# Kernel optimization log

Measured on AMD Instinct MI355X. Metric: run time of the kernel, lower is better.

## Reference

```python
import jax, jax.numpy as jnp
import numpy as np

N_NODES = 100000
N_EDGES = 640000
WIDTH = 128
LAYERS = 3
N_GRAPHS = 64


def setup_inputs() -> dict:
    key = jax.random.key(0)
    ks = jax.random.split(key, 6)
    x = jax.random.normal(ks[0], (N_NODES, WIDTH), dtype=jnp.float32)
    edge_index = jax.random.randint(ks[1], (2, N_EDGES), 0, N_NODES, dtype=jnp.int64)
    edge_attr = jax.random.uniform(ks[2], (N_EDGES, 1), dtype=jnp.float32)
    batch = jnp.sort(jax.random.randint(ks[3], (N_NODES,), 0, N_GRAPHS, dtype=jnp.int64))
    Ws = jax.random.normal(ks[4], (LAYERS, WIDTH, WIDTH), dtype=jnp.float32) / np.sqrt(WIDTH)
    bs = jnp.zeros((LAYERS, WIDTH), dtype=jnp.float32)
    return {"x": x, "edge_index": edge_index, "edge_attr": edge_attr,
            "batch": batch, "Ws": Ws, "bs": bs}


def reference(x, edge_index, edge_attr, batch, Ws, bs):
    N = x.shape[0]
    ew = edge_attr.squeeze()  # [E]
    loop = jnp.arange(N)
    # add self-loops with fill_value=2.0 (improved=True)
    row = jnp.concatenate([edge_index[0], loop])
    col = jnp.concatenate([edge_index[1], loop])
    w = jnp.concatenate([ew, jnp.full((N,), 2.0, dtype=ew.dtype)])
    # symmetric gcn normalization: deg computed at target (col)
    deg = jax.ops.segment_sum(w, col, num_segments=N)
    dinv = jnp.where(deg > 0, jax.lax.rsqrt(deg), 0.0)
    norm = dinv[row] * w * dinv[col]  # [E+N]

    for l in range(LAYERS):
        h = x @ Ws[l]  # [N, WIDTH]
        msg = norm[:, None] * h[row]  # gather + scale
        x = jax.ops.segment_sum(msg, col, num_segments=N) + bs[l]

    # global mean pool over graphs
    sums = jax.ops.segment_sum(x, batch, num_segments=N_GRAPHS)
    counts = jax.ops.segment_sum(jnp.ones((N,), dtype=x.dtype), batch, num_segments=N_GRAPHS)
    return sums / jnp.maximum(counts, 1.0)[:, None]
```

## Files before the change

kernel.cpp:

```cpp
#include <hip/hip_runtime.h>
#include <hip/hip_fp16.h>
#include <cstddef>

#define N_NODES  100000
#define N_EDGES  640000
#define WIDTH    128
#define LAYERS   3
#define N_GRAPHS 64
#define ELL_K    40

__device__ __forceinline__ float h2f(unsigned short h) {
  __half x; *reinterpret_cast<unsigned short*>(&x) = h;
  return __half2float(x);
}
__device__ __forceinline__ unsigned short f2h(float f) {
  __half h = __float2half_rn(f);
  return *reinterpret_cast<unsigned short*>(&h);
}


__global__ void k_init(int* __restrict__ cursor, float* __restrict__ deg) {
  int i = blockIdx.x * blockDim.x + threadIdx.x;
  if (i < N_NODES) { cursor[i] = 0; deg[i] = 0.f; }
}

__global__ void k_fill_cd(const int* __restrict__ row, const int* __restrict__ col,
                          const float* __restrict__ ew,
                          int* __restrict__ cursor, float* __restrict__ deg,
                          int2* __restrict__ ell) {
  int e = blockIdx.x * blockDim.x + threadIdx.x;
  if (e < N_EDGES) {
    int r = row[e], c = col[e];
    float w = ew[e];
    atomicAdd(&deg[c], w);
    int slot = atomicAdd(&cursor[r], 1);
    if (slot < ELL_K) {
      int2 pk; pk.x = c; pk.y = __float_as_int(w);
      ell[(size_t)r * ELL_K + slot] = pk;
    }
  }
}

__global__ void k_dinv_e(const float* __restrict__ deg, float* __restrict__ dinv,
                         float* __restrict__ d2, float* __restrict__ sq) {
  int v = blockIdx.x * blockDim.x + threadIdx.x;
  if (v < N_NODES) {
    float d = 2.0f + deg[v];
    float di = (d > 0.0f) ? 1.0f / sqrtf(d) : 0.0f;
    dinv[v] = di;
    d2[v] = di * di;
    sq[v] = sqrtf(d);
  }
}

__device__ __forceinline__ int lbound(const int* __restrict__ batch, int key) {
  int lo = 0, hi = N_NODES;
  while (lo < hi) { int m = (lo + hi) >> 1; if (batch[m] < key) lo = m + 1; else hi = m; }
  return lo;
}

__global__ void k_cntg(const int* __restrict__ batch, int* __restrict__ cntg,
                       float* __restrict__ invc) {
  int g = threadIdx.x;
  if (g < N_GRAPHS) {
    int lb = lbound(batch, g), ub = lbound(batch, g + 1);
    int c = ub - lb;
    cntg[g] = c;
    invc[g] = 1.0f / (float)max(c, 1);
  }
}

__global__ void k_pinit(const int* __restrict__ batch, const float* __restrict__ invc,
                        const float* __restrict__ dinv, unsigned short* __restrict__ p) {
  const int total = N_NODES * 16;
  for (int i = blockIdx.x * blockDim.x + threadIdx.x; i < total;
       i += gridDim.x * blockDim.x) {
    int v = i >> 4, q = i & 15;
    int b = batch[v];
    unsigned short val = f2h(invc[b] * dinv[v]);
    ushort4 u;
    ((unsigned short*)&u)[0] = (q * 4 + 0 == b) ? val : (unsigned short)0;
    ((unsigned short*)&u)[1] = (q * 4 + 1 == b) ? val : (unsigned short)0;
    ((unsigned short*)&u)[2] = (q * 4 + 2 == b) ? val : (unsigned short)0;
    ((unsigned short*)&u)[3] = (q * 4 + 3 == b) ? val : (unsigned short)0;
    ((ushort4*)p)[i] = u;
  }
}

#define CS_BLOCKS 512
__global__ __launch_bounds__(256) void k_colsum(
    const unsigned short* __restrict__ y, const float* __restrict__ sq,
    float* __restrict__ partc) {
  __shared__ float4 sd[256];
  int t = threadIdx.x;
  int slot = t & 15;
  int vrow = t >> 4;
  const int chunk = (N_NODES + CS_BLOCKS - 1) / CS_BLOCKS;
  int start = blockIdx.x * chunk;
  int end = min(start + chunk, N_NODES);
  float4 acc = {0.f, 0.f, 0.f, 0.f};
  for (int v = start + vrow; v < end; v += 16) {
    ushort4 u = ((const ushort4*)(y + (size_t)v * 64))[slot];
    float rd = sq[v];
    acc.x += h2f(u.x) * rd; acc.y += h2f(u.y) * rd;
    acc.z += h2f(u.z) * rd; acc.w += h2f(u.w) * rd;
  }
  sd[t] = acc;
  __syncthreads();
  for (int off = 8; off > 0; off >>= 1) {
    if (vrow < off) {
      float4 o = sd[(vrow + off) * 16 + slot];
      acc.x += o.x; acc.y += o.y; acc.z += o.z; acc.w += o.w;
      sd[t] = acc;
    }
    __syncthreads();
  }
  if (vrow == 0)
    ((float4*)(partc + (size_t)blockIdx.x * 64))[slot] = acc;
}

__global__ __launch_bounds__(256) void k_cs2(
    const float* __restrict__ csA, const float* __restrict__ csB,
    float* __restrict__ ps, float* __restrict__ pas) {
  __shared__ float sd[256];
  const float* src = (blockIdx.x == 0) ? csA : csB;
  float* dst = (blockIdx.x == 0) ? ps : pas;
  int t = threadIdx.x;
  int g = t & 63, c = t >> 6;
  float a = 0.f;
  for (int r = c * 128; r < (c + 1) * 128; r++) a += src[r * 64 + g];
  sd[t] = a;
  __syncthreads();
  if (t < 128) sd[t] += sd[t + 128];
  __syncthreads();
  if (t < 64) dst[t] = sd[t] + sd[t + 64];
}

#define AGG_NPB 4
__global__ __launch_bounds__(256) void k_yagg(
    const unsigned short* __restrict__ yin, const int* __restrict__ cnt_a,
    const int2* __restrict__ ell, const float* __restrict__ scale,
    unsigned short* __restrict__ yout) {
  int wave = threadIdx.x >> 6;
  int lane = threadIdx.x & 63;
  int v = blockIdx.x * AGG_NPB + wave;
  if (v >= N_NODES) return;
  int vv = __builtin_amdgcn_readfirstlane(v);
  int grp = lane >> 4;
  int q = lane & 15;

  ushort4 hvu = ((const ushort4*)(yin + (size_t)vv * 64))[q];
  int cnt = cnt_a[vv];

  float4 a0 = {0,0,0,0}, a1 = {0,0,0,0}, a2 = {0,0,0,0}, a3 = {0,0,0,0};
  int2 pk = (lane < cnt) ? ell[(size_t)vv * ELL_K + lane] : make_int2(0, 0);
  int   si = pk.x;
  float swv = __int_as_float(pk.y);

  for (int base = 0; base < cnt; base += 16) {
    int e0 = base + grp;
    float w0 = __shfl(swv, e0); int i0 = __shfl(si, e0);
    ushort4 u0 = ((const ushort4*)(yin + (size_t)i0 * 64))[q];
    a0.x += w0 * h2f(u0.x); a0.y += w0 * h2f(u0.y);
    a0.z += w0 * h2f(u0.z); a0.w += w0 * h2f(u0.w);
    if (base + 4 < cnt) {
      int e1 = base + 4 + grp;
      float w1 = __shfl(swv, e1); int i1 = __shfl(si, e1);
      ushort4 u1 = ((const ushort4*)(yin + (size_t)i1 * 64))[q];
      a1.x += w1 * h2f(u1.x); a1.y += w1 * h2f(u1.y);
      a1.z += w1 * h2f(u1.z); a1.w += w1 * h2f(u1.w);
    }
    if (base + 8 < cnt) {
      int e2 = base + 8 + grp;
      int e3 = base + 12 + grp;
      float w2 = __shfl(swv, e2); int i2 = __shfl(si, e2);
      float w3 = __shfl(swv, e3); int i3 = __shfl(si, e3);
      ushort4 u2 = ((const ushort4*)(yin + (size_t)i2 * 64))[q];
      ushort4 u3 = ((const ushort4*)(yin + (size_t)i3 * 64))[q];
      a2.x += w2 * h2f(u2.x); a2.y += w2 * h2f(u2.y);
      a2.z += w2 * h2f(u2.z); a2.w += w2 * h2f(u2.w);
      a3.x += w3 * h2f(u3.x); a3.y += w3 * h2f(u3.y);
      a3.z += w3 * h2f(u3.z); a3.w += w3 * h2f(u3.w);
    }
  }

  a0.x += a1.x + a2.x + a3.x;
  a0.y += a1.y + a2.y + a3.y;
  a0.z += a1.z + a2.z + a3.z;
  a0.w += a1.w + a2.w + a3.w;
#pragma unroll
  for (int d = 16; d <= 32; d <<= 1) {
    a0.x += __shfl_xor(a0.x, d);
    a0.y += __shfl_xor(a0.y, d);
    a0.z += __shfl_xor(a0.z, d);
    a0.w += __shfl_xor(a0.w, d);
  }

  if (grp == 0) {
    float sc = scale[vv];
    ushort4 r;
    r.x = f2h(sc * (a0.x + 2.0f * h2f(hvu.x)));
    r.y = f2h(sc * (a0.y + 2.0f * h2f(hvu.y)));
    r.z = f2h(sc * (a0.z + 2.0f * h2f(hvu.z)));
    r.w = f2h(sc * (a0.w + 2.0f * h2f(hvu.w)));
    ((ushort4*)(yout + (size_t)vv * 64))[q] = r;
  }
}

#define CT_BLOCKS 1024

__global__ __launch_bounds__(256) void k_contract(
    const float* __restrict__ x0, const unsigned short* __restrict__ y3,
    float* __restrict__ part) {
  int t = threadIdx.x;
  int jq = t & 31;
  int gg = t >> 5;

  float4 acc[8];
#pragma unroll
  for (int i = 0; i < 8; i++) acc[i] = make_float4(0.f, 0.f, 0.f, 0.f);

  int v = blockIdx.x;
  for (; v + CT_BLOCKS < N_NODES; v += 2 * CT_BLOCKS) {
    int v2 = v + CT_BLOCKS;
    float4 xa = ((const float4*)(x0 + (size_t)v * WIDTH))[jq];
    float4 xb = ((const float4*)(x0 + (size_t)v2 * WIDTH))[jq];
    const ushort4* ya = (const ushort4*)(y3 + (size_t)v * 64 + gg * 8);
    const ushort4* yb = (const ushort4*)(y3 + (size_t)v2 * 64 + gg * 8);
    ushort4 ua0 = ya[0], ua1 = ya[1];
    ushort4 ub0 = yb[0], ub1 = yb[1];
    float yas[8] = {h2f(ua0.x), h2f(ua0.y), h2f(ua0.z), h2f(ua0.w),
                    h2f(ua1.x), h2f(ua1.y), h2f(ua1.z), h2f(ua1.w)};
    float ybs[8] = {h2f(ub0.x), h2f(ub0.y), h2f(ub0.z), h2f(ub0.w),
                    h2f(ub1.x), h2f(ub1.y), h2f(ub1.z), h2f(ub1.w)};
#pragma unroll
    for (int i = 0; i < 8; i++) {
      acc[i].x += yas[i] * xa.x; acc[i].y += yas[i] * xa.y;
      acc[i].z += yas[i] * xa.z; acc[i].w += yas[i] * xa.w;
    }
#pragma unroll
    for (int i = 0; i < 8; i++) {
      acc[i].x += ybs[i] * xb.x; acc[i].y += ybs[i] * xb.y;
      acc[i].z += ybs[i] * xb.z; acc[i].w += ybs[i] * xb.w;
    }
  }
  if (v < N_NODES) {
    float4 xa = ((const float4*)(x0 + (size_t)v * WIDTH))[jq];
    const ushort4* ya = (const ushort4*)(y3 + (size_t)v * 64 + gg * 8);
    ushort4 ua0 = ya[0], ua1 = ya[1];
    float yas[8] = {h2f(ua0.x), h2f(ua0.y), h2f(ua0.z), h2f(ua0.w),
                    h2f(ua1.x), h2f(ua1.y), h2f(ua1.z), h2f(ua1.w)};
#pragma unroll
    for (int i = 0; i < 8; i++) {
      acc[i].x += yas[i] * xa.x; acc[i].y += yas[i] * xa.y;
      acc[i].z += yas[i] * xa.z; acc[i].w += yas[i] * xa.w;
    }
  }

  float* dst = part + (size_t)blockIdx.x * (N_GRAPHS * WIDTH);
#pragma unroll
  for (int i = 0; i < 8; i++)
    *(float4*)(dst + (gg * 8 + i) * WIDTH + jq * 4) = acc[i];
}

#define RC_ROWS 64
#define RC_RG (CT_BLOCKS / RC_ROWS)

__global__ __launch_bounds__(256) void k_reduce1(
    const float* __restrict__ part, float* __restrict__ part2) {
  int bid = blockIdx.x, t = threadIdx.x;
  int rg = bid >> 5, colc = bid & 31;
  int idx = colc * 256 + t;
  const float* src = part + (size_t)rg * RC_ROWS * (N_GRAPHS * WIDTH) + idx;
  float a0 = 0.f, a1 = 0.f, a2 = 0.f, a3 = 0.f;
  for (int r = 0; r < RC_ROWS; r += 4) {
    a0 += src[(size_t)(r + 0) * (N_GRAPHS * WIDTH)];
    a1 += src[(size_t)(r + 1) * (N_GRAPHS * WIDTH)];
    a2 += src[(size_t)(r + 2) * (N_GRAPHS * WIDTH)];
    a3 += src[(size_t)(r + 3) * (N_GRAPHS * WIDTH)];
  }
  part2[rg * (N_GRAPHS * WIDTH) + idx] = (a0 + a1) + (a2 + a3);
}

__global__ __launch_bounds__(WIDTH) void k_mm128(
    const float* __restrict__ A, const float* __restrict__ B, float* __restrict__ O) {
  __shared__ float Ar[WIDTH];
  int r = blockIdx.x, j = threadIdx.x;
  Ar[j] = A[r * WIDTH + j];
  __syncthreads();
  float a = 0.f;
#pragma unroll 8
  for (int k = 0; k < WIDTH; k++) a += Ar[k] * B[k * WIDTH + j];
  O[r * WIDTH + j] = a;
}

__global__ __launch_bounds__(WIDTH) void k_c01(
    const float* __restrict__ b0, const float* __restrict__ T1,
    const float* __restrict__ b1, const float* __restrict__ W2,
    float* __restrict__ c0, float* __restrict__ c1) {
  __shared__ float s0[WIDTH], s1v[WIDTH];
  int j = threadIdx.x;
  s0[j] = b0[j]; s1v[j] = b1[j];
  __syncthreads();
  float a0 = 0.f, a1 = 0.f;
#pragma unroll 8
  for (int k = 0; k < WIDTH; k++) {
    a0 += s0[k] * T1[k * WIDTH + j];
    a1 += s1v[k] * W2[k * WIDTH + j];
  }
  c0[j] = a0; c1[j] = a1;
}

__global__ __launch_bounds__(WIDTH) void k_out(
    const float* __restrict__ part2, const float* __restrict__ Wp,
    const float* __restrict__ c0, const float* __restrict__ c1,
    const float* __restrict__ ps, const float* __restrict__ pas,
    const int* __restrict__ cntg, const float* __restrict__ b2,
    float* __restrict__ out) {
  __shared__ float Cr[WIDTH];
  int g = blockIdx.x, j = threadIdx.x;
  float cv = 0.f;
#pragma unroll
  for (int rg = 0; rg < RC_RG; rg++)
    cv += part2[rg * (N_GRAPHS * WIDTH) + g * WIDTH + j];
  Cr[j] = cv;
  __syncthreads();
  float a = pas[g] * c0[j] + ps[g] * c1[j] + ((cntg[g] > 0) ? b2[j] : 0.f);
#pragma unroll 8
  for (int k = 0; k < WIDTH; k++) a += Cr[k] * Wp[k * WIDTH + j];
  out[g * WIDTH + j] = a;
}


extern "C" void kernel_launch(void* const* d_in, const int* in_sizes, int n_in,
                              void* d_out, int out_size, void* d_ws, size_t ws_size,
                              hipStream_t stream) {
  const float* x   = (const float*)d_in[0];
  const int* row   = (const int*)d_in[1];
  const int* col   = row + N_EDGES;
  const float* ew  = (const float*)d_in[2];
  const int* batch = (const int*)d_in[3];
  const float* Ws  = (const float*)d_in[4];
  const float* bs  = (const float*)d_in[5];
  float* out = (float*)d_out;

  char* w = (char*)d_ws;
  float* dinv    = (float*)(w + 0);
  float* d2      = (float*)(w + 400128);
  float* sq      = (float*)(w + 800256);
  float* deg     = (float*)(w + 1200384);
  int*   cursor  = (int*)(w + 1600512);
  int*   cntg    = (int*)(w + 2000640);
  float* invc    = (float*)(w + 2000896);
  float* ps      = (float*)(w + 2001152);
  float* pas     = (float*)(w + 2001408);
  float* T1      = (float*)(w + 2001664);
  float* Wp      = (float*)(w + 2067200);
  float* c0      = (float*)(w + 2132736);
  float* c1      = (float*)(w + 2133248);
  int2*  ell     = (int2*)(w + 2133760);
  float* part    = (float*)(w + 34133760);
  float* part2   = (float*)(w + 67688192);
  unsigned short* yA = (unsigned short*)(w + 68212480);
  unsigned short* yB = (unsigned short*)(w + 81012480);
  float* csA     = (float*)(w + 93812480);
  float* csB     = (float*)(w + 93943552);

  int nb_n = (N_NODES + 255) / 256;
  int nb_e = (N_EDGES + 255) / 256;

  k_init   <<<nb_n, 256, 0, stream>>>(cursor, deg);
  k_fill_cd<<<nb_e, 256, 0, stream>>>(row, col, ew, cursor, deg, ell);
  k_dinv_e <<<nb_n, 256, 0, stream>>>(deg, dinv, d2, sq);

  k_cntg <<<1, 64, 0, stream>>>(batch, cntg, invc);
  k_pinit<<<2048, 256, 0, stream>>>(batch, invc, dinv, yA);

  int nb_y = (N_NODES + AGG_NPB - 1) / AGG_NPB;
  k_yagg  <<<nb_y, 256, 0, stream>>>(yA, cursor, ell, d2, yB);
  k_colsum<<<CS_BLOCKS, 256, 0, stream>>>(yB, sq, csA);
  k_yagg  <<<nb_y, 256, 0, stream>>>(yB, cursor, ell, d2, yA);
  k_colsum<<<CS_BLOCKS, 256, 0, stream>>>(yA, sq, csB);
  k_yagg  <<<nb_y, 256, 0, stream>>>(yA, cursor, ell, dinv, yB);

  k_cs2  <<<2, 256, 0, stream>>>(csA, csB, ps, pas);
  k_mm128<<<WIDTH, WIDTH, 0, stream>>>(Ws + 1 * WIDTH * WIDTH, Ws + 2 * WIDTH * WIDTH, T1);
  k_mm128<<<WIDTH, WIDTH, 0, stream>>>(Ws + 0 * WIDTH * WIDTH, T1, Wp);
  k_c01  <<<1, WIDTH, 0, stream>>>(bs, T1, bs + WIDTH, Ws + 2 * WIDTH * WIDTH, c0, c1);

  k_contract<<<CT_BLOCKS, 256, 0, stream>>>(x, yB, part);
  k_reduce1 <<<RC_RG * 32, 256, 0, stream>>>(part, part2);
  k_out     <<<N_GRAPHS, WIDTH, 0, stream>>>(part2, Wp, c0, c1, ps, pas, cntg,
                                             bs + 2 * WIDTH, out);
}
```

Measured before the change: 278.8 us.

## Stage contraction tiles in LDS via direct global-to-LDS loads

Restructures the contraction kernel so each block processes contiguous 64-node chunks. The x rows are loaded straight into shared memory with global_load_lds, and the fp16 y rows are converted to fp32 in shared memory before the FMA loop. Each thread now owns 16 graph-rows by 2 columns instead of 8 by 4, and the grid shrinks to 768 blocks. The aim is coalesced bulk loads and less per-node global traffic and conversion, at the cost of barriers, 48KB of LDS per block and lower occupancy. The reduce kernel's RC_RG still derives from CT_BLOCKS (now 768), so the partial-sum reduction must cope with the new block count.

Result: no change. 274.1 us (-1.7%).

```diff
diff --git a/kernel.cpp b/kernel.cpp
--- a/kernel.cpp
+++ b/kernel.cpp
@@ -8,6 +8,11 @@
 #define LAYERS   3
 #define N_GRAPHS 64
 #define ELL_K    40
+
+#define GLOAD_LDS16(gsrc, ldst) \
+  __builtin_amdgcn_global_load_lds( \
+      (const __attribute__((address_space(1))) unsigned*)(gsrc), \
+      (__attribute__((address_space(3))) unsigned*)(ldst), 16, 0, 0)
 
 __device__ __forceinline__ float h2f(unsigned short h) {
   __half x; *reinterpret_cast<unsigned short*>(&x) = h;
@@ -207,60 +212,93 @@
   }
 }
 
-#define CT_BLOCKS 1024
+#define CT_BLOCKS 768
+#define CT_NCHUNK ((N_NODES + 63) / 64)
 
 __global__ __launch_bounds__(256) void k_contract(
     const float* __restrict__ x0, const unsigned short* __restrict__ y3,
     float* __restrict__ part) {
+  __shared__ __align__(16) float xs[64 * 128];
+  __shared__ __align__(16) float ysf[64 * 64];
   int t = threadIdx.x;
-  int jq = t & 31;
-  int gg = t >> 5;
-
-  float4 acc[8];
-#pragma unroll
-  for (int i = 0; i < 8; i++) acc[i] = make_float4(0.f, 0.f, 0.f, 0.f);
-
-  int v = blockIdx.x;
-  for (; v + CT_BLOCKS < N_NODES; v += 2 * CT_BLOCKS) {
-    int v2 = v + CT_BLOCKS;
-    float4 xa = ((const float4*)(x0 + (size_t)v * WIDTH))[jq];
-    float4 xb = ((const float4*)(x0 + (size_t)v2 * WIDTH))[jq];
-    const ushort4* ya = (const ushort4*)(y3 + (size_t)v * 64 + gg * 8);
-    const ushort4* yb = (const ushort4*)(y3 + (size_t)v2 * 64 + gg * 8);
-    ushort4 ua0 = ya[0], ua1 = ya[1];
-    ushort4 ub0 = yb[0], ub1 = yb[1];
-    float yas[8] = {h2f(ua0.x), h2f(ua0.y), h2f(ua0.z), h2f(ua0.w),
-                    h2f(ua1.x), h2f(ua1.y), h2f(ua1.z), h2f(ua1.w)};
-    float ybs[8] = {h2f(ub0.x), h2f(ub0.y), h2f(ub0.z), h2f(ub0.w),
-                    h2f(ub1.x), h2f(ub1.y), h2f(ub1.z), h2f(ub1.w)};
+  int w = t >> 6;
+  int lane = t & 63;
+  int j = lane * 2;
+
+  float2 acc[16];
+#pragma unroll
+  for (int i = 0; i < 16; i++) acc[i] = make_float2(0.f, 0.f);
+
+  for (int c = blockIdx.x; c < CT_NCHUNK; c += gridDim.x) {
+    int cc = min(64, N_NODES - c * 64);
+    int bx = cc * 512;
+    int byh = cc * 128;
+    const char* gx = (const char*)(x0 + (size_t)c * 64 * 128);
+    const char* gy = (const char*)(y3 + (size_t)c * 64 * 64);
+    __syncthreads();
 #pragma unroll
     for (int i = 0; i < 8; i++) {
-      acc[i].x += yas[i] * xa.x; acc[i].y += yas[i] * xa.y;
-      acc[i].z += yas[i] * xa.z; acc[i].w += yas[i] * xa.w;
-    }
-#pragma unroll
-    for (int i = 0; i < 8; i++) {
-      acc[i].x += ybs[i] * xb.x; acc[i].y += ybs[i] * xb.y;
-      acc[i].z += ybs[i] * xb.z; acc[i].w += ybs[i] * xb.w;
-    }
-  }
-  if (v < N_NODES) {
-    float4 xa = ((const float4*)(x0 + (size_t)v * WIDTH))[jq];
-    const ushort4* ya = (const ushort4*)(y3 + (size_t)v * 64 + gg * 8);
-    ushort4 ua0 = ya[0], ua1 = ya[1];
-    float yas[8] = {h2f(ua0.x), h2f(ua0.y), h2f(ua0.z), h2f(ua0.w),
-                    h2f(ua1.x), h2f(ua1.y), h2f(ua1.z), h2f(ua1.w)};
-#pragma unroll
-    for (int i = 0; i < 8; i++) {
-      acc[i].x += yas[i] * xa.x; acc[i].y += yas[i] * xa.y;
-      acc[i].z += yas[i] * xa.z; acc[i].w += yas[i] * xa.w;
+      int off = i * 4096 + t * 16;
+      if (off < bx) GLOAD_LDS16(gx + off, (char*)xs + off);
+    }
+    ushort4 u[4];
+#pragma unroll
+    for (int r = 0; r < 4; r++) {
+      int off = (r * 256 + t) * 8;
+      u[r] = (off < byh) ? *(const ushort4*)(gy + off)
+                         : make_ushort4(0, 0, 0, 0);
+    }
+#pragma unroll
+    for (int r = 0; r < 4; r++) {
+      int idx = (r * 256 + t) * 4;
+      if (idx < cc * 64)
+        *(float4*)(ysf + idx) = make_float4(h2f(u[r].x), h2f(u[r].y),
+                                            h2f(u[r].z), h2f(u[r].w));
+    }
+    asm volatile("s_waitcnt vmcnt(0)" ::: "memory");
+    __syncthreads();
+
+    int v = 0;
+    for (; v + 2 <= cc; v += 2) {
+      float2 xa = *(const float2*)(xs + v * 128 + j);
+      float2 xb = *(const float2*)(xs + (v + 1) * 128 + j);
+      const float4* ya = (const float4*)(ysf + v * 64 + w * 16);
+      const float4* yb = (const float4*)(ysf + (v + 1) * 64 + w * 16);
+      float4 a0 = ya[0], a1 = ya[1], a2 = ya[2], a3 = ya[3];
+      float4 b0 = yb[0], b1 = yb[1], b2 = yb[2], b3 = yb[3];
+      float yas[16] = {a0.x, a0.y, a0.z, a0.w, a1.x, a1.y, a1.z, a1.w,
+                       a2.x, a2.y, a2.z, a2.w, a3.x, a3.y, a3.z, a3.w};
+      float ybs[16] = {b0.x, b0.y, b0.z, b0.w, b1.x, b1.y, b1.z, b1.w,
+                       b2.x, b2.y, b2.z, b2.w, b3.x, b3.y, b3.z, b3.w};
+#pragma unroll
+      for (int i = 0; i < 16; i++) {
+        acc[i].x += yas[i] * xa.x;
+        acc[i].y += yas[i] * xa.y;
+      }
+#pragma unroll
+      for (int i = 0; i < 16; i++) {
+        acc[i].x += ybs[i] * xb.x;
+        acc[i].y += ybs[i] * xb.y;
+      }
+    }
+    if (v < cc) {
+      float2 xa = *(const float2*)(xs + v * 128 + j);
+      const float4* ya = (const float4*)(ysf + v * 64 + w * 16);
+      float4 a0 = ya[0], a1 = ya[1], a2 = ya[2], a3 = ya[3];
+      float yas[16] = {a0.x, a0.y, a0.z, a0.w, a1.x, a1.y, a1.z, a1.w,
+                       a2.x, a2.y, a2.z, a2.w, a3.x, a3.y, a3.z, a3.w};
+#pragma unroll
+      for (int i = 0; i < 16; i++) {
+        acc[i].x += yas[i] * xa.x;
+        acc[i].y += yas[i] * xa.y;
+      }
     }
   }
 
   float* dst = part + (size_t)blockIdx.x * (N_GRAPHS * WIDTH);
 #pragma unroll
-  for (int i = 0; i < 8; i++)
-    *(float4*)(dst + (gg * 8 + i) * WIDTH + jq * 4) = acc[i];
+  for (int i = 0; i < 16; i++)
+    *(float2*)(dst + (w * 16 + i) * WIDTH + j) = acc[i];
 }
 
 #define RC_ROWS 64
```
